# Performance work log

Hardware: AMD Instinct MI355X
Metric: run time of the kernel (lower is better)

## Reference

```python
import jax, jax.numpy as jnp
from jax import lax
import numpy as np

HIDDEN = 512
WINDOW = 24
KERNEL = 3
BATCH = 2048
OUT = 1
STDV = 1.0 / np.sqrt(HIDDEN)


def setup_inputs() -> dict:
    key = jax.random.key(0)
    ks = jax.random.split(key, 16)
    u = lambda k, shape: jax.random.uniform(k, shape, jnp.float32, -STDV, STDV)
    L = HIDDEN + KERNEL - 1  # conv 'valid' output length must equal HIDDEN
    return {
        "Z": jax.random.normal(ks[0], (2, BATCH, L), jnp.float32),
        "d": jax.random.normal(ks[1], (1, BATCH, HIDDEN), jnp.float32),
        "s": jax.random.normal(ks[2], (1, BATCH, HIDDEN), jnp.float32),
        "y_real": jax.random.normal(ks[3], (BATCH, WINDOW), jnp.float32),
        "vd": u(ks[4], (HIDDEN,)),
        "Wd": u(ks[5], (HIDDEN, 2 * HIDDEN)),
        "Ud": u(ks[6], (HIDDEN, HIDDEN)),
        "w": u(ks[7], (OUT, HIDDEN + WINDOW)),
        "b": u(ks[8], (OUT, 1)),
        "conv_w": u(ks[9], (WINDOW, 2, KERNEL)),  # Conv1d(2, window, kernel)
        "conv_b": u(ks[10], (WINDOW,)),
        "Wih": u(ks[11], (4 * HIDDEN, OUT)),  # LSTM(input=1, hidden)
        "Whh": u(ks[12], (4 * HIDDEN, HIDDEN)),
        "bih": u(ks[13], (4 * HIDDEN,)),
        "bhh": u(ks[14], (4 * HIDDEN,)),
    }


def _forward(Z, d, s, y_real, vd, Wd, Ud, w, b, conv_w, conv_b, Wih, Whh, bih, bhh):
    # conv over Z.transpose(1,0): [B, 2, L] -> H [B, WINDOW, HIDDEN]
    x = jnp.transpose(Z, (1, 0, 2))
    H = lax.conv_general_dilated(x, conv_w, (1,), "VALID",
                                 dimension_numbers=("NCH", "OIH", "NCH"))
    H = jax.nn.relu(H + conv_b[None, :, None])

    d0, s0 = d[0], s[0]  # [B, h] LSTM (h, c) states
    ct0 = jnp.zeros((BATCH, HIDDEN), Z.dtype)

    def step(carry, Hi):  # Hi: [B, HIDDEN]
        d0, s0, ct = carry
        ds = jnp.concatenate([d0, s0], axis=1)  # [B, 2h]
        l = jnp.tanh(ds @ Wd.T + Hi @ Ud.T) @ vd  # [B]
        Bw = jax.nn.softmax(l)  # softmax over batch (dim=1 of [1,B])
        ct = ct + Bw @ Hi  # [h] broadcast-added to [B, h]
        y_fake = jnp.concatenate([y_real, ct], axis=1) @ w[0] + b[0, 0]  # [B]
        # single LSTM cell step, input_size = 1
        gates = y_fake[:, None] @ Wih.T + bih + d0 @ Whh.T + bhh  # [B, 4h]
        ig, fg, gg, og = jnp.split(gates, 4, axis=1)
        s0 = jax.nn.sigmoid(fg) * s0 + jax.nn.sigmoid(ig) * jnp.tanh(gg)
        d0 = jax.nn.sigmoid(og) * jnp.tanh(s0)
        return (d0, s0, ct), y_fake

    (d0, s0, _), ys = lax.scan(step, (d0, s0, ct0), jnp.swapaxes(H, 0, 1))
    y_fake = ys[-1][:, None]  # [B, 1]
    return y_fake, (d0[None], s0[None])


def reference(Z, d, s, y_real, vd, Wd, Ud, w, b, conv_w, conv_b, Wih, Whh, bih, bhh):
    return _forward(Z, d, s, y_real, vd, Wd, Ud, w, b, conv_w, conv_b, Wih, Whh, bih, bhh)
```

## Files before the change

### kernel.cpp

```cpp
#include <hip/hip_runtime.h>
#include <math.h>

#define HIDDEN 512
#define WINDOW 24
#define KSZ 3
#define BATCH 2048
#define L_IN 514
#define H4 2048
#define LDT 40
#define BH (BATCH * HIDDEN)

typedef short short8 __attribute__((ext_vector_type(8)));
typedef float floatx4 __attribute__((ext_vector_type(4)));

__device__ __forceinline__ floatx4 mfma16(short8 a, short8 b, floatx4 c) {
    return __builtin_amdgcn_mfma_f32_16x16x32_bf16(a, b, c, 0, 0, 0);
}
__device__ __forceinline__ unsigned short f2bf(float x) {
    union { float f; unsigned u; } v; v.f = x;
    unsigned r = v.u + 0x7fff + ((v.u >> 16) & 1);
    return (unsigned short)(r >> 16);
}
__device__ __forceinline__ float bf2f(unsigned short u) {
    union { unsigned u; float f; } v; v.u = ((unsigned)u) << 16;
    return v.f;
}
__device__ __forceinline__ float sigmoidf(float x) { return 1.f / (1.f + expf(-x)); }

__device__ __forceinline__ void gload_lds16(const void* g, void* l) {
    __builtin_amdgcn_global_load_lds(
        (const __attribute__((address_space(1))) void*)g,
        (__attribute__((address_space(3))) void*)l, 16, 0, 0);
}

__global__ void cvt5_kernel(const float* __restrict__ s0, unsigned short* __restrict__ d0,
                            const float* __restrict__ s1, unsigned short* __restrict__ d1,
                            const float* __restrict__ s2, unsigned short* __restrict__ d2,
                            const float* __restrict__ s3, unsigned short* __restrict__ d3,
                            const float* __restrict__ s4, unsigned short* __restrict__ d4,
                            const float* __restrict__ y_real, const float* __restrict__ w,
                            float* __restrict__ yr_dot, float* __restrict__ Sacc,
                            int* __restrict__ flags, float* __restrict__ ctwA) {
    const int g = blockIdx.x * blockDim.x + threadIdx.x;
    if (g >= 983040) {
        const int tid = g - 983040;
        if (tid < BATCH) {
            float s = 0.f;
#pragma unroll
            for (int j = 0; j < WINDOW; ++j) s += y_real[tid * WINDOW + j] * w[j];
            yr_dot[tid] = s;
        }
        if (tid < 2 * WINDOW) Sacc[tid] = 0.f;
        if (tid < WINDOW) flags[tid] = 0;
        if (tid == 0) ctwA[0] = 0.f;
        return;
    }
    const float* src; unsigned short* dst; int off, offd;
    if      (g < 131072) { src = s0; dst = d0; off = g; offd = off; }
    else if (g < 196608) { src = s1; dst = d1; off = g - 131072; offd = off; }
    else if (g < 458752) {
        src = s2; dst = d2; off = g - 196608;
        const int row = off >> 7, seg = off & 127;
        const int gg = row >> 9, ii = row & 511;
        const int drow = ((ii >> 4) << 6) + (gg << 4) + (ii & 15);
        offd = drow * 128 + seg;
    }
    else if (g < 720896) { src = s3; dst = d3; off = g - 458752; offd = off; }
    else                 { src = s4; dst = d4; off = g - 720896; offd = off; }
    float4 v = ((const float4*)src)[off];
    uint2 u;
    u.x = (unsigned)f2bf(v.x) | ((unsigned)f2bf(v.y) << 16);
    u.y = (unsigned)f2bf(v.z) | ((unsigned)f2bf(v.w) << 16);
    ((uint2*)dst)[offd] = u;
}

__global__ void conv_kernel(const float* __restrict__ Z, const float* __restrict__ conv_w,
                            const float* __restrict__ conv_b,
                            unsigned int* __restrict__ Htu,
                            const float* __restrict__ w, float* __restrict__ hw) {
    __shared__ float cw[WINDOW * 6];
    __shared__ float cb[WINDOW];
    __shared__ float sm[WINDOW][4];
    const int b = blockIdx.x;
    if (threadIdx.x < WINDOW * 6) cw[threadIdx.x] = conv_w[threadIdx.x];
    if (threadIdx.x < WINDOW) cb[threadIdx.x] = conv_b[threadIdx.x];
    __syncthreads();
    const float* z0 = Z + (size_t)b * L_IN;
    const float* z1 = z0 + (size_t)BATCH * L_IN;
    const int i0 = threadIdx.x * 2;
    const int wave = threadIdx.x >> 6;
    const float a0 = z0[i0], a1 = z0[i0 + 1], a2 = z0[i0 + 2], a3 = z0[i0 + 3];
    const float c0 = z1[i0], c1 = z1[i0 + 1], c2 = z1[i0 + 2], c3 = z1[i0 + 3];
    const float wv0 = w[WINDOW + i0], wv1 = w[WINDOW + i0 + 1];
#pragma unroll
    for (int o = 0; o < WINDOW; ++o) {
        const float* wc = cw + o * 6;
        float v0 = fmaxf(cb[o] + a0 * wc[0] + a1 * wc[1] + a2 * wc[2]
                               + c0 * wc[3] + c1 * wc[4] + c2 * wc[5], 0.f);
        float v1 = fmaxf(cb[o] + a1 * wc[0] + a2 * wc[1] + a3 * wc[2]
                               + c1 * wc[3] + c2 * wc[4] + c3 * wc[5], 0.f);
        const unsigned short h0 = f2bf(v0), h1 = f2bf(v1);
        Htu[((size_t)o * BATCH + b) * 256 + threadIdx.x] =
            (unsigned)h0 | ((unsigned)h1 << 16);
        float c = bf2f(h0) * wv0 + bf2f(h1) * wv1;
#pragma unroll
        for (int m = 1; m < 64; m <<= 1) c += __shfl_xor(c, m, 64);
        if ((threadIdx.x & 63) == 0) sm[o][wave] = c;
    }
    __syncthreads();
    if (threadIdx.x < WINDOW)
        hw[(size_t)threadIdx.x * BATCH + b] =
            sm[threadIdx.x][0] + sm[threadIdx.x][1] + sm[threadIdx.x][2] + sm[threadIdx.x][3];
}

__global__ __launch_bounds__(256) void g_gemm_mfma(const unsigned short* __restrict__ Htb,
                                                   const unsigned short* __restrict__ Udb,
                                                   unsigned short* __restrict__ Gb) {
    __shared__ __align__(16) short As[2 * 8 * 512];
    __shared__ __align__(16) short Bs[2 * 8 * 512];
    const int blk = blockIdx.x;
    const int xcd = blk & 7;
    const int grp = blk >> 3;
    const int nt  = grp & 3;
    const int mt  = (grp >> 2) * 8 + xcd;
    const int tid = threadIdx.x;
    const int wave = tid >> 6, lane = tid & 63;
    const int wm = wave >> 1, wn = wave & 1;
    const int quad = lane >> 4, lr = lane & 15;
    const int m0 = mt * 128, n0 = nt * 128;
    const int wr = lane >> 2;
    const int ws = (lane & 3) ^ (lane >> 4);
    const int rsw = (lr * 4 + (quad ^ (lr >> 2))) * 8;
    floatx4 acc[4][4] = {};
    for (int k0 = 0; k0 < HIDDEN; k0 += 64) {
#pragma unroll
        for (int c8 = 0; c8 < 8; ++c8) {
            const int cc = wave * 8 + c8;
            const int cc2 = cc & 15;
            const int h = cc2 >> 3, ch = cc2 & 7;
            if (cc < 16)
                gload_lds16(Htb + (size_t)(m0 + ch * 16 + wr) * HIDDEN + k0 + 32 * h + ws * 8,
                            As + (h * 8 + ch) * 512);
            else
                gload_lds16(Udb + (size_t)(n0 + ch * 16 + wr) * HIDDEN + k0 + 32 * h + ws * 8,
                            Bs + (h * 8 + ch) * 512);
        }
        __syncthreads();
#pragma unroll
        for (int h = 0; h < 2; ++h) {
            short8 a[4], bv[4];
#pragma unroll
            for (int f = 0; f < 4; ++f) {
                a[f]  = *(const short8*)(As + (h * 8 + wm * 4 + f) * 512 + rsw);
                bv[f] = *(const short8*)(Bs + (h * 8 + wn * 4 + f) * 512 + rsw);
            }
#pragma unroll
            for (int mf = 0; mf < 4; ++mf)
#pragma unroll
                for (int nf = 0; nf < 4; ++nf)
                    acc[mf][nf] = mfma16(a[mf], bv[nf], acc[mf][nf]);
        }
        __syncthreads();
    }
#pragma unroll
    for (int mf = 0; mf < 4; ++mf)
#pragma unroll
        for (int nf = 0; nf < 4; ++nf)
#pragma unroll
            for (int r = 0; r < 4; ++r) {
                const int m = m0 + wm * 64 + mf * 16 + quad * 4 + r;
                const int n = n0 + wn * 64 + nf * 16 + lr;
                Gb[(size_t)m * HIDDEN + n] = f2bf(acc[mf][nf][r]);
            }
}

__global__ __launch_bounds__(256) void s1_mfma(const unsigned short* __restrict__ db,
                                               const unsigned short* __restrict__ sb,
                                               const unsigned short* __restrict__ Wdb,
                                               const unsigned short* __restrict__ Gtb,
                                               const float* __restrict__ vd,
                                               float* __restrict__ lpart) {
    __shared__ __align__(16) short Asd[2][64 * LDT];
    __shared__ __align__(16) short Ass[2][64 * LDT];
    __shared__ __align__(16) short Bsd[2][32 * LDT];
    __shared__ __align__(16) short Bss[2][32 * LDT];
    __shared__ float red[2][64];
    const int tid = threadIdx.x;
    const int wave = tid >> 6, lane = tid & 63;
    const int wm = wave >> 1, wn = wave & 1;
    const int quad = lane >> 4, lr = lane & 15, qk = quad * 8;
    const int m0 = (blockIdx.x & 31) * 64;
    const int nb = blockIdx.x >> 5;
    const int n0 = nb * 32;
    const int arow = tid >> 2, aseg = tid & 3;
    floatx4 accd[2] = {}, accs[2] = {};
    for (int k0 = 0; k0 < HIDDEN; k0 += 64) {
#pragma unroll
        for (int h = 0; h < 2; ++h) {
            const int kk = k0 + 32 * h;
            *(float4*)(Asd[h] + arow * LDT + aseg * 8) =
                *(const float4*)(db + (size_t)(m0 + arow) * HIDDEN + kk + aseg * 8);
            *(float4*)(Ass[h] + arow * LDT + aseg * 8) =
                *(const float4*)(sb + (size_t)(m0 + arow) * HIDDEN + kk + aseg * 8);
            const int r2 = tid & 127, brow = r2 >> 2, bseg = r2 & 3;
            short* dst = (tid < 128) ? Bsd[h] : Bss[h];
            const int coff = (tid < 128) ? 0 : HIDDEN;
            *(float4*)(dst + brow * LDT + bseg * 8) =
                *(const float4*)(Wdb + (size_t)(n0 + brow) * (2 * HIDDEN) + coff + kk + bseg * 8);
        }
        __syncthreads();
#pragma unroll
        for (int h = 0; h < 2; ++h) {
            short8 ad0 = *(const short8*)(Asd[h] + (wm * 32 + lr) * LDT + qk);
            short8 ad1 = *(const short8*)(Asd[h] + (wm * 32 + 16 + lr) * LDT + qk);
            short8 as0 = *(const short8*)(Ass[h] + (wm * 32 + lr) * LDT + qk);
            short8 as1 = *(const short8*)(Ass[h] + (wm * 32 + 16 + lr) * LDT + qk);
            short8 bd  = *(const short8*)(Bsd[h] + (wn * 16 + lr) * LDT + qk);
            short8 bs  = *(const short8*)(Bss[h] + (wn * 16 + lr) * LDT + qk);
            accd[0] = mfma16(ad0, bd, accd[0]);
            accd[1] = mfma16(ad1, bd, accd[1]);
            accs[0] = mfma16(as0, bs, accs[0]);
            accs[1] = mfma16(as1, bs, accs[1]);
        }
        __syncthreads();
    }
#pragma unroll
    for (int mf = 0; mf < 2; ++mf) {
        float rs[4];
#pragma unroll
        for (int r = 0; r < 4; ++r) {
            const int b = m0 + wm * 32 + mf * 16 + quad * 4 + r;
            const int i = n0 + wn * 16 + lr;
            float v = tanhf(accd[mf][r] + accs[mf][r] + bf2f(Gtb[(size_t)b * HIDDEN + i])) * vd[i];
            for (int msk = 1; msk < 16; msk <<= 1) v += __shfl_xor(v, msk, 16);
            rs[r] = v;
        }
        if (lr == 0)
#pragma unroll
            for (int r = 0; r < 4; ++r)
                red[wn][wm * 32 + mf * 16 + quad * 4 + r] = rs[r];
    }
    __syncthreads();
    if (tid < 64)
        lpart[(size_t)nb * BATCH + m0 + tid] = red[0][tid] + red[1][tid];
}

__global__ __launch_bounds__(256) void gates_lstm_mfma(
        const unsigned short* __restrict__ db, const unsigned short* __restrict__ Whhb,
        const float* __restrict__ Wih, const float* __restrict__ bih,
        const float* __restrict__ bhh, const float* __restrict__ yr_dot,
        const float* __restrict__ lpart, const float* __restrict__ hw_t,
        float* __restrict__ Sacc, int* __restrict__ flags,
        float* __restrict__ ctwA, const float* __restrict__ b00,
        const float* __restrict__ s_old, float* __restrict__ s_new,
        float* __restrict__ d_new,
        unsigned short* __restrict__ sb_new, unsigned short* __restrict__ db_new,
        float* __restrict__ y_out, int t) {
    __shared__ __align__(16) short As[4 * 4 * 512];
    __shared__ __align__(16) short Bs[4 * 8 * 512];
    __shared__ float sSe[2];
    const int tid = threadIdx.x;
    const int wave = tid >> 6, lane = tid & 63;
    const int wm = wave >> 1, wn = wave & 1;
    const int quad = lane >> 4, lr = lane & 15;
    const int mt = blockIdx.x & 31, nt = blockIdx.x >> 5;
    const int m0 = mt * 64, n0 = nt * 128;

    if (nt == 0 && tid < 64) {
        const int b = m0 + tid;
        float l = 0.f;
#pragma unroll
        for (int p = 0; p < 16; ++p) l += lpart[(size_t)p * BATCH + b];
        float e = expf(l);
        float eh = e * hw_t[b];
#pragma unroll
        for (int m = 1; m < 64; m <<= 1) {
            e  += __shfl_xor(e, m, 64);
            eh += __shfl_xor(eh, m, 64);
        }
        if (tid == 0) {
            __hip_atomic_fetch_add(&Sacc[2 * t], e, __ATOMIC_RELAXED, __HIP_MEMORY_SCOPE_AGENT);
            __hip_atomic_fetch_add(&Sacc[2 * t + 1], eh, __ATOMIC_RELAXED, __HIP_MEMORY_SCOPE_AGENT);
        }
    }
    __syncthreads();
    if (nt == 0 && tid == 0)
        __hip_atomic_fetch_add(&flags[t], 1, __ATOMIC_RELEASE, __HIP_MEMORY_SCOPE_AGENT);

    const int wr = lane >> 2;
    const int ws = (lane & 3) ^ (lane >> 4);
    const int rsw = (lr * 4 + (quad ^ (lr >> 2))) * 8;

    floatx4 acc[2][4] = {};
    for (int k0 = 0; k0 < HIDDEN; k0 += 128) {
#pragma unroll
        for (int wi = 0; wi < 12; ++wi) {
            const int h = wave;
            const int kk = k0 + 32 * h;
            if (wi < 4)
                gload_lds16(db + (size_t)(m0 + wi * 16 + wr) * HIDDEN + kk + ws * 8,
                            As + (h * 4 + wi) * 512);
            else {
                const int ch = wi - 4;
                gload_lds16(Whhb + (size_t)(n0 + ch * 16 + wr) * HIDDEN + kk + ws * 8,
                            Bs + (h * 8 + ch) * 512);
            }
        }
        __syncthreads();
#pragma unroll
        for (int h = 0; h < 4; ++h) {
            short8 a0 = *(const short8*)(As + (h * 4 + 2 * wm) * 512 + rsw);
            short8 a1 = *(const short8*)(As + (h * 4 + 2 * wm + 1) * 512 + rsw);
#pragma unroll
            for (int f = 0; f < 4; ++f) {
                short8 bv = *(const short8*)(Bs + (h * 8 + wn * 4 + f) * 512 + rsw);
                acc[0][f] = mfma16(a0, bv, acc[0][f]);
                acc[1][f] = mfma16(a1, bv, acc[1][f]);
            }
        }
        __syncthreads();
    }

    if (tid == 0) {
        while (__hip_atomic_load(&flags[t], __ATOMIC_ACQUIRE, __HIP_MEMORY_SCOPE_AGENT) < 32)
            __builtin_amdgcn_s_sleep(2);
        sSe[0] = __hip_atomic_load(&Sacc[2 * t], __ATOMIC_RELAXED, __HIP_MEMORY_SCOPE_AGENT);
        sSe[1] = __hip_atomic_load(&Sacc[2 * t + 1], __ATOMIC_RELAXED, __HIP_MEMORY_SCOPE_AGENT);
    }
    __syncthreads();
    const float ctw = ctwA[t] + sSe[1] / sSe[0];
    const float ys = ctw + b00[0];
    if (blockIdx.x == 0 && tid == 0) ctwA[t + 1] = ctw;
    if (y_out != nullptr && nt == 0 && tid < 64)
        y_out[m0 + tid] = yr_dot[m0 + tid] + ys;

    const int i = ((n0 + wn * 64) >> 2) + lr;
    float wi4[4], cbv[4];
#pragma unroll
    for (int g = 0; g < 4; ++g) {
        wi4[g] = Wih[g * HIDDEN + i];
        cbv[g] = bih[g * HIDDEN + i] + bhh[g * HIDDEN + i];
    }
#pragma unroll
    for (int mf = 0; mf < 2; ++mf)
#pragma unroll
        for (int r = 0; r < 4; ++r) {
            const int b = m0 + wm * 32 + mf * 16 + quad * 4 + r;
            const float yf = yr_dot[b] + ys;
            const size_t idx = (size_t)b * HIDDEN + i;
            const float ig = acc[mf][0][r] + yf * wi4[0] + cbv[0];
            const float fg = acc[mf][1][r] + yf * wi4[1] + cbv[1];
            const float gg = acc[mf][2][r] + yf * wi4[2] + cbv[2];
            const float og = acc[mf][3][r] + yf * wi4[3] + cbv[3];
            const float sn = sigmoidf(fg) * s_old[idx] + sigmoidf(ig) * tanhf(gg);
            const float dn = sigmoidf(og) * tanhf(sn);
            s_new[idx] = sn;
            sb_new[idx] = f2bf(sn);
            db_new[idx] = f2bf(dn);
            if (d_new != nullptr) d_new[idx] = dn;
        }
}

extern "C" void kernel_launch(void* const* d_in, const int* in_sizes, int n_in,
                              void* d_out, int out_size, void* d_ws, size_t ws_size,
                              hipStream_t stream) {
    const float* Z      = (const float*)d_in[0];
    const float* d_init = (const float*)d_in[1];
    const float* s_init = (const float*)d_in[2];
    const float* y_real = (const float*)d_in[3];
    const float* vd     = (const float*)d_in[4];
    const float* Wd     = (const float*)d_in[5];
    const float* Ud     = (const float*)d_in[6];
    const float* w      = (const float*)d_in[7];
    const float* b00    = (const float*)d_in[8];
    const float* conv_w = (const float*)d_in[9];
    const float* conv_b = (const float*)d_in[10];
    const float* Wih    = (const float*)d_in[11];
    const float* Whh    = (const float*)d_in[12];
    const float* bih    = (const float*)d_in[13];
    const float* bhh    = (const float*)d_in[14];

    float* ws = (float*)d_ws;
    size_t off = 0;
    unsigned short* Htb = (unsigned short*)(ws + off);  off += (size_t)WINDOW * BH / 2;
    unsigned short* Gb  = (unsigned short*)(ws + off);  off += (size_t)WINDOW * BH / 2;
    unsigned short* dbb[2];
    dbb[0] = (unsigned short*)(ws + off);  off += BH / 2;
    dbb[1] = (unsigned short*)(ws + off);  off += BH / 2;
    unsigned short* sbb[2];
    sbb[0] = (unsigned short*)(ws + off);  off += BH / 2;
    sbb[1] = (unsigned short*)(ws + off);  off += BH / 2;
    float* sbuf[2];
    sbuf[0] = ws + off;  off += BH;
    sbuf[1] = ws + off;  off += BH;
    unsigned short* Wdb  = (unsigned short*)(ws + off);  off += (size_t)HIDDEN * 2 * HIDDEN / 2;
    unsigned short* Udb  = (unsigned short*)(ws + off);  off += (size_t)HIDDEN * HIDDEN / 2;
    unsigned short* Whhb = (unsigned short*)(ws + off);  off += (size_t)H4 * HIDDEN / 2;
    float* hw     = ws + off;  off += (size_t)WINDOW * BATCH;
    float* lpart  = ws + off;  off += (size_t)16 * BATCH;
    float* yr_dot = ws + off;  off += BATCH;
    float* Sacc   = ws + off;  off += 2 * WINDOW;
    float* ctwA   = ws + off;  off += WINDOW + 4;
    int*   flags  = (int*)(ws + off);  off += WINDOW;

    float* out = (float*)d_out;
    float* y_out   = out;
    float* d_out_f = out + BATCH;
    float* s_out_f = out + BATCH + (size_t)BH;

    cvt5_kernel<<<3848, 256, 0, stream>>>(Wd, Wdb, Ud, Udb, Whh, Whhb,
                                          d_init, dbb[0], s_init, sbb[0],
                                          y_real, w, yr_dot, Sacc, flags, ctwA);
    conv_kernel<<<BATCH, 256, 0, stream>>>(Z, conv_w, conv_b, (unsigned int*)Htb, w, hw);
    g_gemm_mfma<<<384 * 4, 256, 0, stream>>>(Htb, Udb, Gb);

    const float* s_read = s_init;
    int pp = 0;
    for (int t = 0; t < WINDOW; ++t) {
        const unsigned short* Gtb = Gb + (size_t)t * BH;
        s1_mfma<<<512, 256, 0, stream>>>(dbb[pp], sbb[pp], Wdb, Gtb, vd, lpart);
        const bool last = (t == WINDOW - 1);
        float* s_w = last ? s_out_f : sbuf[t & 1];
        float* d_w = last ? d_out_f : nullptr;
        float* y_w = last ? y_out : nullptr;
        gates_lstm_mfma<<<512, 256, 0, stream>>>(dbb[pp], Whhb, Wih, bih, bhh, yr_dot,
                                                 lpart, hw + t * BATCH, Sacc, flags,
                                                 ctwA, b00, s_read, s_w, d_w,
                                                 sbb[1 - pp], dbb[1 - pp], y_w, t);
        s_read = s_w;
        pp ^= 1;
    }
}
```

Before: 855.3 us.

## Use direct global-to-LDS loads with swizzled layout in s1 attention GEMM

Rewrites the s1_mfma staging to load tiles straight from global memory into LDS through a gload_lds16 helper, with each wave loading one 32-wide K slice. It uses an XOR-swizzled 16-row block layout in place of padded rows and processes 128 K per barrier instead of 64. This halves the number of syncs and avoids the register round trip and LDS bank conflicts. LDS use grows, which may lower occupancy, and correctness depends on the helper and swizzle matching the MFMA fragment reads.

```diff
diff --git a/kernel.cpp b/kernel.cpp
--- a/kernel.cpp
+++ b/kernel.cpp
@@ -180,43 +180,50 @@
                                                const unsigned short* __restrict__ Gtb,
                                                const float* __restrict__ vd,
                                                float* __restrict__ lpart) {
-    __shared__ __align__(16) short Asd[2][64 * LDT];
-    __shared__ __align__(16) short Ass[2][64 * LDT];
-    __shared__ __align__(16) short Bsd[2][32 * LDT];
-    __shared__ __align__(16) short Bss[2][32 * LDT];
+    __shared__ __align__(16) short Asd[4 * 4 * 512];
+    __shared__ __align__(16) short Ass[4 * 4 * 512];
+    __shared__ __align__(16) short Bsd[4 * 2 * 512];
+    __shared__ __align__(16) short Bss[4 * 2 * 512];
     __shared__ float red[2][64];
     const int tid = threadIdx.x;
     const int wave = tid >> 6, lane = tid & 63;
     const int wm = wave >> 1, wn = wave & 1;
-    const int quad = lane >> 4, lr = lane & 15, qk = quad * 8;
+    const int quad = lane >> 4, lr = lane & 15;
     const int m0 = (blockIdx.x & 31) * 64;
     const int nb = blockIdx.x >> 5;
     const int n0 = nb * 32;
-    const int arow = tid >> 2, aseg = tid & 3;
+    const int wr = lane >> 2;
+    const int ws = (lane & 3) ^ (lane >> 4);
+    const int rsw = (lr * 4 + (quad ^ (lr >> 2))) * 8;
+
     floatx4 accd[2] = {}, accs[2] = {};
-    for (int k0 = 0; k0 < HIDDEN; k0 += 64) {
-#pragma unroll
-        for (int h = 0; h < 2; ++h) {
-            const int kk = k0 + 32 * h;
-            *(float4*)(Asd[h] + arow * LDT + aseg * 8) =
-                *(const float4*)(db + (size_t)(m0 + arow) * HIDDEN + kk + aseg * 8);
-            *(float4*)(Ass[h] + arow * LDT + aseg * 8) =
-                *(const float4*)(sb + (size_t)(m0 + arow) * HIDDEN + kk + aseg * 8);
-            const int r2 = tid & 127, brow = r2 >> 2, bseg = r2 & 3;
-            short* dst = (tid < 128) ? Bsd[h] : Bss[h];
-            const int coff = (tid < 128) ? 0 : HIDDEN;
-            *(float4*)(dst + brow * LDT + bseg * 8) =
-                *(const float4*)(Wdb + (size_t)(n0 + brow) * (2 * HIDDEN) + coff + kk + bseg * 8);
-        }
-        __syncthreads();
-#pragma unroll
-        for (int h = 0; h < 2; ++h) {
-            short8 ad0 = *(const short8*)(Asd[h] + (wm * 32 + lr) * LDT + qk);
-            short8 ad1 = *(const short8*)(Asd[h] + (wm * 32 + 16 + lr) * LDT + qk);
-            short8 as0 = *(const short8*)(Ass[h] + (wm * 32 + lr) * LDT + qk);
-            short8 as1 = *(const short8*)(Ass[h] + (wm * 32 + 16 + lr) * LDT + qk);
-            short8 bd  = *(const short8*)(Bsd[h] + (wn * 16 + lr) * LDT + qk);
-            short8 bs  = *(const short8*)(Bss[h] + (wn * 16 + lr) * LDT + qk);
+    for (int k0 = 0; k0 < HIDDEN; k0 += 128) {
+        const int h = wave;
+        const int kk = k0 + 32 * h;
+#pragma unroll
+        for (int wi = 0; wi < 12; ++wi) {
+            if (wi < 4)
+                gload_lds16(db + (size_t)(m0 + wi * 16 + wr) * HIDDEN + kk + ws * 8,
+                            Asd + (h * 4 + wi) * 512);
+            else if (wi < 8)
+                gload_lds16(sb + (size_t)(m0 + (wi - 4) * 16 + wr) * HIDDEN + kk + ws * 8,
+                            Ass + (h * 4 + (wi - 4)) * 512);
+            else if (wi < 10)
+                gload_lds16(Wdb + (size_t)(n0 + (wi - 8) * 16 + wr) * (2 * HIDDEN) + kk + ws * 8,
+                            Bsd + (h * 2 + (wi - 8)) * 512);
+            else
+                gload_lds16(Wdb + (size_t)(n0 + (wi - 10) * 16 + wr) * (2 * HIDDEN) + HIDDEN + kk + ws * 8,
+                            Bss + (h * 2 + (wi - 10)) * 512);
+        }
+        __syncthreads();
+#pragma unroll
+        for (int hh = 0; hh < 4; ++hh) {
+            short8 ad0 = *(const short8*)(Asd + (hh * 4 + 2 * wm) * 512 + rsw);
+            short8 ad1 = *(const short8*)(Asd + (hh * 4 + 2 * wm + 1) * 512 + rsw);
+            short8 as0 = *(const short8*)(Ass + (hh * 4 + 2 * wm) * 512 + rsw);
+            short8 as1 = *(const short8*)(Ass + (hh * 4 + 2 * wm + 1) * 512 + rsw);
+            short8 bd  = *(const short8*)(Bsd + (hh * 2 + wn) * 512 + rsw);
+            short8 bs  = *(const short8*)(Bss + (hh * 2 + wn) * 512 + rsw);
             accd[0] = mfma16(ad0, bd, accd[0]);
             accd[1] = mfma16(ad1, bd, accd[1]);
             accs[0] = mfma16(as0, bs, accs[0]);
```

Result: faster. 807.0 us (-5.6%).
